# Kernel tuning notes

Measured on AMD Instinct MI355X. Metric: run time of the kernel, lower is better.

Reference implementation:

```python
import jax, jax.numpy as jnp
import numpy as np

N = 2048
EMBED_DIM = 64
N_SUBJ, N_REL, N_OBJ = 16, 9, 16


def setup_inputs() -> dict:
    key = jax.random.key(0)
    ks = jax.random.split(key, 16)
    scale = 0.05  # keep sigmoid unsaturated
    return {
        "subj_idx": jax.random.randint(ks[0], (N,), 0, N_SUBJ, dtype=jnp.int32),
        "rel_idx": jax.random.randint(ks[1], (N,), 0, N_REL, dtype=jnp.int32),
        "obj_idx": jax.random.randint(ks[2], (N,), 0, N_OBJ, dtype=jnp.int32),
        "subj_table": jax.random.normal(ks[3], (N_SUBJ, EMBED_DIM), jnp.float32),
        "rel_table": jax.random.normal(ks[4], (N_REL, EMBED_DIM), jnp.float32),
        "obj_table": jax.random.normal(ks[5], (N_OBJ, EMBED_DIM), jnp.float32),
        "proj_w": jax.random.normal(ks[6], (EMBED_DIM, 3 * EMBED_DIM), jnp.float32) * scale,
        "proj_b": jax.random.normal(ks[7], (EMBED_DIM,), jnp.float32) * scale,
        "w1": jax.random.normal(ks[8], (EMBED_DIM, 2 * EMBED_DIM), jnp.float32) * scale,
        "b1": jax.random.normal(ks[9], (EMBED_DIM,), jnp.float32) * scale,
        "w2": jax.random.normal(ks[10], (32, EMBED_DIM), jnp.float32) * scale,
        "b2": jax.random.normal(ks[11], (32,), jnp.float32) * scale,
        "w3": jax.random.normal(ks[12], (1, 32), jnp.float32) * scale,
        "b3": jax.random.normal(ks[13], (1,), jnp.float32) * scale,
    }


def reference(subj_idx, rel_idx, obj_idx, subj_table, rel_table, obj_table,
              proj_w, proj_b, w1, b1, w2, b2, w3, b3):
    # --- ClaimEmbedder.embed, batched over all N claims ---
    # combined [N, 3*D] = cat(subj, rel, obj) embeddings; proj -> [N, D]
    combined = jnp.concatenate(
        [subj_table[subj_idx], rel_table[rel_idx], obj_table[obj_idx]], axis=-1)
    e = combined @ proj_w.T + proj_b  # [N, D]

    # --- conflict_scorer over all ordered pairs (i, j) ---
    # Linear(2D -> D) on cat(e_i, e_j) == e_i @ W1a.T + e_j @ W1b.T + b1
    d = e.shape[-1]
    w1a, w1b = w1[:, :d], w1[:, d:]
    hi = e @ w1a.T          # [N, D] contribution of left claim
    hj = e @ w1b.T          # [N, D] contribution of right claim
    h = jax.nn.relu(hi[:, None, :] + hj[None, :, :] + b1)  # [N, N, D]
    # Dropout(0.1) is identity in eval / no_grad inference.
    h2 = jax.nn.relu(jnp.einsum('ijd,kd->ijk', h, w2) + b2)  # [N, N, 32]
    scores = jax.nn.sigmoid(jnp.einsum('ijk,k->ij', h2, w3[0]) + b3[0])  # [N, N]
    # Only pairs with i < j are scored in the original nested loop.
    return jnp.triu(scores, k=1)
```

## Files before the change

### kernel.cpp

```cpp
#include <hip/hip_runtime.h>
#include <hip/hip_bf16.h>

#define NROWS 2048
#define HH 72

typedef __attribute__((ext_vector_type(4))) float f32x4;
typedef _Float16 f16x2 __attribute__((ext_vector_type(2)));
typedef _Float16 f16x8 __attribute__((ext_vector_type(8)));
typedef __fp16 fp16x2_raw __attribute__((ext_vector_type(2)));

union H8 { f16x8 v; f16x2 h2[4]; };

static __device__ __forceinline__ f32x4 vmax0(f32x4 a) {
    return __builtin_elementwise_max(a, (f32x4)0.f);
}
static __device__ __forceinline__ f16x8 hmax0(f16x8 a) {
    return __builtin_elementwise_max(a, (f16x8)(_Float16)0.f);
}
static __device__ __forceinline__ f16x2 pkrtz(float a, float b) {
    union { fp16x2_raw r; f16x2 f; } c;
    c.r = __builtin_amdgcn_cvt_pkrtz(a, b);
    return c.f;
}

#define TJ_OFF   2688
#define H16_OFF  5376

__global__ __launch_bounds__(256) void tab_kernel(
    const float* __restrict__ subj_table, const float* __restrict__ rel_table,
    const float* __restrict__ obj_table,
    const float* __restrict__ proj_w, const float* __restrict__ proj_b,
    const float* __restrict__ w1, const float* __restrict__ b1,
    float* __restrict__ ws)
{
    __shared__ float et[64];
    const int b = blockIdx.x;
    const int side = b & 1;
    const int r = b >> 1;
    const int tid = threadIdx.x;
    const int lane = tid & 63;
    const int w = tid >> 6;

    if (r == 41) {
        if (tid < 64) et[tid] = proj_b[tid];
    } else {
        const float* src; int off;
        if (r < 16)      { src = subj_table + r * 64;        off = 0;   }
        else if (r < 25) { src = rel_table + (r - 16) * 64;  off = 64;  }
        else             { src = obj_table + (r - 25) * 64;  off = 128; }
        const float sv = src[lane];
        #pragma unroll
        for (int t = 0; t < 4; ++t) {
            const int d0 = w * 16 + t * 4;
            float p0 = sv * proj_w[(d0 + 0) * 192 + off + lane];
            float p1 = sv * proj_w[(d0 + 1) * 192 + off + lane];
            float p2 = sv * proj_w[(d0 + 2) * 192 + off + lane];
            float p3 = sv * proj_w[(d0 + 3) * 192 + off + lane];
            #pragma unroll
            for (int m = 1; m < 64; m <<= 1) {
                p0 += __shfl_xor(p0, m, 64);
                p1 += __shfl_xor(p1, m, 64);
                p2 += __shfl_xor(p2, m, 64);
                p3 += __shfl_xor(p3, m, 64);
            }
            if (lane == 0) {
                et[d0 + 0] = p0; et[d0 + 1] = p1;
                et[d0 + 2] = p2; et[d0 + 3] = p3;
            }
        }
    }
    __syncthreads();

    float* dst = ws + (side ? TJ_OFF : 0);
    const float sv2 = et[lane];
    const int woff = side * 64;
    #pragma unroll
    for (int t = 0; t < 4; ++t) {
        const int d0 = w * 16 + t * 4;
        float p0 = sv2 * w1[(d0 + 0) * 128 + woff + lane];
        float p1 = sv2 * w1[(d0 + 1) * 128 + woff + lane];
        float p2 = sv2 * w1[(d0 + 2) * 128 + woff + lane];
        float p3 = sv2 * w1[(d0 + 3) * 128 + woff + lane];
        #pragma unroll
        for (int m = 1; m < 64; m <<= 1) {
            p0 += __shfl_xor(p0, m, 64);
            p1 += __shfl_xor(p1, m, 64);
            p2 += __shfl_xor(p2, m, 64);
            p3 += __shfl_xor(p3, m, 64);
        }
        if (lane == 0) {
            const bool cst = (side == 0) && (r == 41);
            dst[r * 64 + d0 + 0] = p0 + (cst ? b1[d0 + 0] : 0.f);
            dst[r * 64 + d0 + 1] = p1 + (cst ? b1[d0 + 1] : 0.f);
            dst[r * 64 + d0 + 2] = p2 + (cst ? b1[d0 + 2] : 0.f);
            dst[r * 64 + d0 + 3] = p3 + (cst ? b1[d0 + 3] : 0.f);
        }
    }
}

__global__ __launch_bounds__(256) void hgather_kernel(
    const int* __restrict__ subj_idx, const int* __restrict__ rel_idx,
    const int* __restrict__ obj_idx, float* __restrict__ ws)
{
    _Float16* hi16 = (_Float16*)(ws + H16_OFF);
    _Float16* hj16 = hi16 + NROWS * 64;
    const float* TI = ws;
    const float* TJ = ws + TJ_OFF;

    const int t = threadIdx.x;
    const int n = blockIdx.x * 32 + (t >> 3);
    const int c = (t & 7) * 8;

    const int s = subj_idx[n];
    const int r = 16 + rel_idx[n];
    const int o = 25 + obj_idx[n];

    const f32x4 v0 = *(const f32x4*)(TI + s * 64 + c)
                   + *(const f32x4*)(TI + r * 64 + c)
                   + *(const f32x4*)(TI + o * 64 + c)
                   + *(const f32x4*)(TI + 41 * 64 + c);
    const f32x4 v1 = *(const f32x4*)(TI + s * 64 + c + 4)
                   + *(const f32x4*)(TI + r * 64 + c + 4)
                   + *(const f32x4*)(TI + o * 64 + c + 4)
                   + *(const f32x4*)(TI + 41 * 64 + c + 4);
    H8 hp;
    hp.h2[0] = pkrtz(v0[0], v0[1]); hp.h2[1] = pkrtz(v0[2], v0[3]);
    hp.h2[2] = pkrtz(v1[0], v1[1]); hp.h2[3] = pkrtz(v1[2], v1[3]);
    *(f16x8*)&hi16[(size_t)n * 64 + c] = hp.v;

    const f32x4 u0 = *(const f32x4*)(TJ + s * 64 + c)
                   + *(const f32x4*)(TJ + r * 64 + c)
                   + *(const f32x4*)(TJ + o * 64 + c)
                   + *(const f32x4*)(TJ + 41 * 64 + c);
    const f32x4 u1 = *(const f32x4*)(TJ + s * 64 + c + 4)
                   + *(const f32x4*)(TJ + r * 64 + c + 4)
                   + *(const f32x4*)(TJ + o * 64 + c + 4)
                   + *(const f32x4*)(TJ + 41 * 64 + c + 4);
    H8 hq;
    hq.h2[0] = pkrtz(u0[0], u0[1]); hq.h2[1] = pkrtz(u0[2], u0[3]);
    hq.h2[2] = pkrtz(u1[0], u1[1]); hq.h2[3] = pkrtz(u1[2], u1[3]);
    *(f16x8*)&hj16[(size_t)n * 64 + c] = hq.v;
}

__global__ __launch_bounds__(256) void zfill_kernel(float* __restrict__ out)
{
    const int bid = blockIdx.x;
    int by = (int)((1.f + sqrtf(1.f + 8.f * (float)bid)) * 0.5f);
    while (by * (by - 1) / 2 > bid) --by;
    while ((by + 1) * by / 2 <= bid) ++by;
    const int bx = bid - by * (by - 1) / 2;
    const int i0 = by * 32, j0 = bx * 32;
    const int t = threadIdx.x;
    const int r = t >> 3, c = (t & 7) * 4;
    const float4 z = {0.f, 0.f, 0.f, 0.f};
    *(float4*)(out + (size_t)(i0 + r) * NROWS + j0 + c) = z;
}

#define PSTR2 132

__global__ __launch_bounds__(256, 4) void pair_kernel(
    const float* __restrict__ ws,
    const float* __restrict__ w2, const float* __restrict__ b2,
    const float* __restrict__ w3, const float* __restrict__ b3,
    float* __restrict__ out)
{
    const int bid = blockIdx.x;
    int by = (int)((129.f - sqrtf(16641.f - 8.f * (float)bid)) * 0.5f);
    while (by * (129 - by) / 2 > bid) --by;
    while ((by + 1) * (129 - (by + 1)) / 2 <= bid) ++by;
    const int bx = by + (bid - by * (129 - by) / 2);
    const int i0 = by * 32, j0 = bx * 32;
    const int tid = threadIdx.x;

    __shared__ _Float16 hiL[32 * HH];
    __shared__ _Float16 hjL[32 * HH];
    __shared__ float part[4 * 8 * PSTR2];

    const _Float16* hi16 = (const _Float16*)(ws + H16_OFF);
    const _Float16* hj16 = hi16 + NROWS * 64;

    const int lane = tid & 63;
    const int wi   = tid >> 6;
    const int col  = lane & 15;
    const int quad = lane >> 4;

    {
        const int rr = tid >> 3;
        const int cc = (tid & 7) * 8;
        *(f16x8*)&hiL[rr * HH + cc] = *(const f16x8*)(hi16 + (size_t)(i0 + rr) * 64 + cc);
        *(f16x8*)&hjL[rr * HH + cc] = *(const f16x8*)(hj16 + (size_t)(j0 + rr) * 64 + cc);
    }

    H8 wf[2][2];
    #pragma unroll
    for (int ch = 0; ch < 2; ++ch)
        #pragma unroll
        for (int ks = 0; ks < 2; ++ks) {
            const f32x4* wr = (const f32x4*)(w2 + (ch * 16 + col) * 64 + ks * 32 + quad * 8);
            const f32x4 w0 = wr[0], w1v = wr[1];
            wf[ch][ks].h2[0] = pkrtz(w0[0], w0[1]);
            wf[ch][ks].h2[1] = pkrtz(w0[2], w0[3]);
            wf[ch][ks].h2[2] = pkrtz(w1v[0], w1v[1]);
            wf[ch][ks].h2[3] = pkrtz(w1v[2], w1v[3]);
        }
    const f32x4 b2A = *(const f32x4*)(b2 + quad * 4);
    const f32x4 b2B = *(const f32x4*)(b2 + 16 + quad * 4);
    const f32x4 w3A = *(const f32x4*)(w3 + quad * 4);
    const f32x4 w3B = *(const f32x4*)(w3 + 16 + quad * 4);
    const float b3v = b3[0];

    __syncthreads();

    const int hjb0 = (col) * HH + quad * 8;
    const int hjb1 = (16 + col) * HH + quad * 8;
    const f16x8 hj00 = *(const f16x8*)&hjL[hjb0];
    const f16x8 hj01 = *(const f16x8*)&hjL[hjb0 + 32];
    const f16x8 hj10 = *(const f16x8*)&hjL[hjb1];
    const f16x8 hj11 = *(const f16x8*)&hjL[hjb1 + 32];

    float* mypart = &part[wi * 8 * PSTR2];

    #pragma unroll
    for (int it = 0; it < 8; ++it) {
        const int base = (wi * 8 + it) * HH + quad * 8;
        const f16x8 x0 = *(const f16x8*)&hiL[base];
        const f16x8 x1 = *(const f16x8*)&hiL[base + 32];

        const f16x8 f00 = hmax0(x0 + hj00);
        const f16x8 f01 = hmax0(x1 + hj01);
        const f16x8 f10 = hmax0(x0 + hj10);
        const f16x8 f11 = hmax0(x1 + hj11);

        f32x4 a0 = __builtin_amdgcn_mfma_f32_16x16x32_f16(wf[0][0].v, f00, b2A, 0, 0, 0);
        f32x4 b0 = __builtin_amdgcn_mfma_f32_16x16x32_f16(wf[1][0].v, f00, b2B, 0, 0, 0);
        f32x4 a1 = __builtin_amdgcn_mfma_f32_16x16x32_f16(wf[0][0].v, f10, b2A, 0, 0, 0);
        f32x4 b1 = __builtin_amdgcn_mfma_f32_16x16x32_f16(wf[1][0].v, f10, b2B, 0, 0, 0);
        a0 = __builtin_amdgcn_mfma_f32_16x16x32_f16(wf[0][1].v, f01, a0, 0, 0, 0);
        b0 = __builtin_amdgcn_mfma_f32_16x16x32_f16(wf[1][1].v, f01, b0, 0, 0, 0);
        a1 = __builtin_amdgcn_mfma_f32_16x16x32_f16(wf[0][1].v, f11, a1, 0, 0, 0);
        b1 = __builtin_amdgcn_mfma_f32_16x16x32_f16(wf[1][1].v, f11, b1, 0, 0, 0);

        const f32x4 t0 = vmax0(a0) * w3A + vmax0(b0) * w3B;
        const f32x4 t1 = vmax0(a1) * w3A + vmax0(b1) * w3B;
        mypart[it * PSTR2 +      quad * 16 + col] = (t0[0] + t0[1]) + (t0[2] + t0[3]);
        mypart[it * PSTR2 + 64 + quad * 16 + col] = (t1[0] + t1[1]) + (t1[2] + t1[3]);
    }

    {
        const int itx = lane >> 3;
        const int jc  = (lane & 7) * 4;
        const int g   = jc >> 4;
        const int c4  = jc & 15;
        const float* pr = &mypart[itx * PSTR2 + g * 64 + c4];
        const f32x4 s = *(const f32x4*)(pr)
                      + *(const f32x4*)(pr + 16)
                      + *(const f32x4*)(pr + 32)
                      + *(const f32x4*)(pr + 48);
        const int i  = i0 + wi * 8 + itx;
        const int jb = j0 + jc;
        float4 o;
        o.x = (jb + 0 > i) ? 1.f / (1.f + __expf(-(s[0] + b3v))) : 0.f;
        o.y = (jb + 1 > i) ? 1.f / (1.f + __expf(-(s[1] + b3v))) : 0.f;
        o.z = (jb + 2 > i) ? 1.f / (1.f + __expf(-(s[2] + b3v))) : 0.f;
        o.w = (jb + 3 > i) ? 1.f / (1.f + __expf(-(s[3] + b3v))) : 0.f;
        *(float4*)(out + (size_t)i * NROWS + jb) = o;
    }
}

extern "C" void kernel_launch(void* const* d_in, const int* in_sizes, int n_in,
                              void* d_out, int out_size, void* d_ws, size_t ws_size,
                              hipStream_t stream) {
    const int*   subj_idx   = (const int*)d_in[0];
    const int*   rel_idx    = (const int*)d_in[1];
    const int*   obj_idx    = (const int*)d_in[2];
    const float* subj_table = (const float*)d_in[3];
    const float* rel_table  = (const float*)d_in[4];
    const float* obj_table  = (const float*)d_in[5];
    const float* proj_w     = (const float*)d_in[6];
    const float* proj_b     = (const float*)d_in[7];
    const float* w1         = (const float*)d_in[8];
    const float* b1         = (const float*)d_in[9];
    const float* w2         = (const float*)d_in[10];
    const float* b2         = (const float*)d_in[11];
    const float* w3         = (const float*)d_in[12];
    const float* b3         = (const float*)d_in[13];
    float* out = (float*)d_out;
    float* ws  = (float*)d_ws;

    zfill_kernel<<<dim3(2016), dim3(256), 0, stream>>>(out);

    tab_kernel<<<dim3(84), dim3(256), 0, stream>>>(
        subj_table, rel_table, obj_table, proj_w, proj_b, w1, b1, ws);

    hgather_kernel<<<dim3(NROWS / 32), dim3(256), 0, stream>>>(
        subj_idx, rel_idx, obj_idx, ws);

    pair_kernel<<<dim3(2080), dim3(256), 0, stream>>>(
        ws, w2, b2, w3, b3, out);
}
```

Measured before the change: 111.9 us.

## Make pair kernel persistent over tiles with register-prefetched next tile

The pair kernel launches 512 blocks instead of 2080, and each block loops over 4 or 5 upper-triangular tiles. It prefetches the next tile's hi/hj rows into registers while computing the current one. This amortizes the per-block weight setup (w2 conversion, bias loads) and hides global load latency, and the launch bound drops to 2 blocks per SM. The cost is extra __syncthreads per tile and fewer blocks to balance load across CUs.

```diff
diff --git a/kernel.cpp b/kernel.cpp
--- a/kernel.cpp
+++ b/kernel.cpp
@@ -21,6 +21,14 @@
     union { fp16x2_raw r; f16x2 f; } c;
     c.r = __builtin_amdgcn_cvt_pkrtz(a, b);
     return c.f;
+}
+
+static __device__ __forceinline__ void decode_tile(int t, int& oby, int& obx) {
+    int b = (int)((129.f - sqrtf(16641.f - 8.f * (float)t)) * 0.5f);
+    while (b * (129 - b) / 2 > t) --b;
+    while ((b + 1) * (129 - (b + 1)) / 2 <= t) ++b;
+    oby = b;
+    obx = b + (t - b * (129 - b) / 2);
 }
 
 #define TJ_OFF   2688
@@ -158,19 +166,15 @@
 
 #define PSTR2 132
 
-__global__ __launch_bounds__(256, 4) void pair_kernel(
+__global__ __launch_bounds__(256, 2) void pair_kernel(
     const float* __restrict__ ws,
     const float* __restrict__ w2, const float* __restrict__ b2,
     const float* __restrict__ w3, const float* __restrict__ b3,
     float* __restrict__ out)
 {
-    const int bid = blockIdx.x;
-    int by = (int)((129.f - sqrtf(16641.f - 8.f * (float)bid)) * 0.5f);
-    while (by * (129 - by) / 2 > bid) --by;
-    while ((by + 1) * (129 - (by + 1)) / 2 <= bid) ++by;
-    const int bx = by + (bid - by * (129 - by) / 2);
-    const int i0 = by * 32, j0 = bx * 32;
+    const int blk = blockIdx.x;
     const int tid = threadIdx.x;
+    const int ntile = 4 + (blk < 32);
 
     __shared__ _Float16 hiL[32 * HH];
     __shared__ _Float16 hjL[32 * HH];
@@ -183,13 +187,8 @@
     const int wi   = tid >> 6;
     const int col  = lane & 15;
     const int quad = lane >> 4;
-
-    {
-        const int rr = tid >> 3;
-        const int cc = (tid & 7) * 8;
-        *(f16x8*)&hiL[rr * HH + cc] = *(const f16x8*)(hi16 + (size_t)(i0 + rr) * 64 + cc);
-        *(f16x8*)&hjL[rr * HH + cc] = *(const f16x8*)(hj16 + (size_t)(j0 + rr) * 64 + cc);
-    }
+    const int rr   = tid >> 3;
+    const int cc   = (tid & 7) * 8;
 
     H8 wf[2][2];
     #pragma unroll
@@ -209,61 +208,83 @@
     const f32x4 w3B = *(const f32x4*)(w3 + 16 + quad * 4);
     const float b3v = b3[0];
 
-    __syncthreads();
-
-    const int hjb0 = (col) * HH + quad * 8;
-    const int hjb1 = (16 + col) * HH + quad * 8;
-    const f16x8 hj00 = *(const f16x8*)&hjL[hjb0];
-    const f16x8 hj01 = *(const f16x8*)&hjL[hjb0 + 32];
-    const f16x8 hj10 = *(const f16x8*)&hjL[hjb1];
-    const f16x8 hj11 = *(const f16x8*)&hjL[hjb1 + 32];
-
     float* mypart = &part[wi * 8 * PSTR2];
 
-    #pragma unroll
-    for (int it = 0; it < 8; ++it) {
-        const int base = (wi * 8 + it) * HH + quad * 8;
-        const f16x8 x0 = *(const f16x8*)&hiL[base];
-        const f16x8 x1 = *(const f16x8*)&hiL[base + 32];
-
-        const f16x8 f00 = hmax0(x0 + hj00);
-        const f16x8 f01 = hmax0(x1 + hj01);
-        const f16x8 f10 = hmax0(x0 + hj10);
-        const f16x8 f11 = hmax0(x1 + hj11);
-
-        f32x4 a0 = __builtin_amdgcn_mfma_f32_16x16x32_f16(wf[0][0].v, f00, b2A, 0, 0, 0);
-        f32x4 b0 = __builtin_amdgcn_mfma_f32_16x16x32_f16(wf[1][0].v, f00, b2B, 0, 0, 0);
-        f32x4 a1 = __builtin_amdgcn_mfma_f32_16x16x32_f16(wf[0][0].v, f10, b2A, 0, 0, 0);
-        f32x4 b1 = __builtin_amdgcn_mfma_f32_16x16x32_f16(wf[1][0].v, f10, b2B, 0, 0, 0);
-        a0 = __builtin_amdgcn_mfma_f32_16x16x32_f16(wf[0][1].v, f01, a0, 0, 0, 0);
-        b0 = __builtin_amdgcn_mfma_f32_16x16x32_f16(wf[1][1].v, f01, b0, 0, 0, 0);
-        a1 = __builtin_amdgcn_mfma_f32_16x16x32_f16(wf[0][1].v, f11, a1, 0, 0, 0);
-        b1 = __builtin_amdgcn_mfma_f32_16x16x32_f16(wf[1][1].v, f11, b1, 0, 0, 0);
-
-        const f32x4 t0 = vmax0(a0) * w3A + vmax0(b0) * w3B;
-        const f32x4 t1 = vmax0(a1) * w3A + vmax0(b1) * w3B;
-        mypart[it * PSTR2 +      quad * 16 + col] = (t0[0] + t0[1]) + (t0[2] + t0[3]);
-        mypart[it * PSTR2 + 64 + quad * 16 + col] = (t1[0] + t1[1]) + (t1[2] + t1[3]);
-    }
-
-    {
-        const int itx = lane >> 3;
-        const int jc  = (lane & 7) * 4;
-        const int g   = jc >> 4;
-        const int c4  = jc & 15;
-        const float* pr = &mypart[itx * PSTR2 + g * 64 + c4];
-        const f32x4 s = *(const f32x4*)(pr)
-                      + *(const f32x4*)(pr + 16)
-                      + *(const f32x4*)(pr + 32)
-                      + *(const f32x4*)(pr + 48);
-        const int i  = i0 + wi * 8 + itx;
-        const int jb = j0 + jc;
-        float4 o;
-        o.x = (jb + 0 > i) ? 1.f / (1.f + __expf(-(s[0] + b3v))) : 0.f;
-        o.y = (jb + 1 > i) ? 1.f / (1.f + __expf(-(s[1] + b3v))) : 0.f;
-        o.z = (jb + 2 > i) ? 1.f / (1.f + __expf(-(s[2] + b3v))) : 0.f;
-        o.w = (jb + 3 > i) ? 1.f / (1.f + __expf(-(s[3] + b3v))) : 0.f;
-        *(float4*)(out + (size_t)i * NROWS + jb) = o;
+    int by, bx;
+    decode_tile(blk * 4, by, bx);
+    f16x8 hiR = *(const f16x8*)(hi16 + (size_t)(by * 32 + rr) * 64 + cc);
+    f16x8 hjR = *(const f16x8*)(hj16 + (size_t)(bx * 32 + rr) * 64 + cc);
+
+    for (int tt = 0; tt < ntile; ++tt) {
+        *(f16x8*)&hiL[rr * HH + cc] = hiR;
+        *(f16x8*)&hjL[rr * HH + cc] = hjR;
+        __syncthreads();
+
+        const int i0 = by * 32, j0 = bx * 32;
+
+        int nby = by, nbx = bx;
+        if (tt + 1 < ntile) {
+            const int tnext = (tt + 1 < 4) ? blk * 4 + tt + 1 : 2048 + blk;
+            decode_tile(tnext, nby, nbx);
+            hiR = *(const f16x8*)(hi16 + (size_t)(nby * 32 + rr) * 64 + cc);
+            hjR = *(const f16x8*)(hj16 + (size_t)(nbx * 32 + rr) * 64 + cc);
+        }
+
+        const int hjb0 = (col) * HH + quad * 8;
+        const int hjb1 = (16 + col) * HH + quad * 8;
+        const f16x8 hj00 = *(const f16x8*)&hjL[hjb0];
+        const f16x8 hj01 = *(const f16x8*)&hjL[hjb0 + 32];
+        const f16x8 hj10 = *(const f16x8*)&hjL[hjb1];
+        const f16x8 hj11 = *(const f16x8*)&hjL[hjb1 + 32];
+
+        #pragma unroll
+        for (int it = 0; it < 8; ++it) {
+            const int base = (wi * 8 + it) * HH + quad * 8;
+            const f16x8 x0 = *(const f16x8*)&hiL[base];
+            const f16x8 x1 = *(const f16x8*)&hiL[base + 32];
+
+            const f16x8 f00 = hmax0(x0 + hj00);
+            const f16x8 f01 = hmax0(x1 + hj01);
+            const f16x8 f10 = hmax0(x0 + hj10);
+            const f16x8 f11 = hmax0(x1 + hj11);
+
+            f32x4 a0 = __builtin_amdgcn_mfma_f32_16x16x32_f16(wf[0][0].v, f00, b2A, 0, 0, 0);
+            f32x4 b0 = __builtin_amdgcn_mfma_f32_16x16x32_f16(wf[1][0].v, f00, b2B, 0, 0, 0);
+            f32x4 a1 = __builtin_amdgcn_mfma_f32_16x16x32_f16(wf[0][0].v, f10, b2A, 0, 0, 0);
+            f32x4 b1 = __builtin_amdgcn_mfma_f32_16x16x32_f16(wf[1][0].v, f10, b2B, 0, 0, 0);
+            a0 = __builtin_amdgcn_mfma_f32_16x16x32_f16(wf[0][1].v, f01, a0, 0, 0, 0);
+            b0 = __builtin_amdgcn_mfma_f32_16x16x32_f16(wf[1][1].v, f01, b0, 0, 0, 0);
+            a1 = __builtin_amdgcn_mfma_f32_16x16x32_f16(wf[0][1].v, f11, a1, 0, 0, 0);
+            b1 = __builtin_amdgcn_mfma_f32_16x16x32_f16(wf[1][1].v, f11, b1, 0, 0, 0);
+
+            const f32x4 t0 = vmax0(a0) * w3A + vmax0(b0) * w3B;
+            const f32x4 t1 = vmax0(a1) * w3A + vmax0(b1) * w3B;
+            mypart[it * PSTR2 +      quad * 16 + col] = (t0[0] + t0[1]) + (t0[2] + t0[3]);
+            mypart[it * PSTR2 + 64 + quad * 16 + col] = (t1[0] + t1[1]) + (t1[2] + t1[3]);
+        }
+
+        {
+            const int itx = lane >> 3;
+            const int jc  = (lane & 7) * 4;
+            const int g   = jc >> 4;
+            const int c4  = jc & 15;
+            const float* pr = &mypart[itx * PSTR2 + g * 64 + c4];
+            const f32x4 s = *(const f32x4*)(pr)
+                          + *(const f32x4*)(pr + 16)
+                          + *(const f32x4*)(pr + 32)
+                          + *(const f32x4*)(pr + 48);
+            const int i  = i0 + wi * 8 + itx;
+            const int jb = j0 + jc;
+            float4 o;
+            o.x = (jb + 0 > i) ? 1.f / (1.f + __expf(-(s[0] + b3v))) : 0.f;
+            o.y = (jb + 1 > i) ? 1.f / (1.f + __expf(-(s[1] + b3v))) : 0.f;
+            o.z = (jb + 2 > i) ? 1.f / (1.f + __expf(-(s[2] + b3v))) : 0.f;
+            o.w = (jb + 3 > i) ? 1.f / (1.f + __expf(-(s[3] + b3v))) : 0.f;
+            *(float4*)(out + (size_t)i * NROWS + jb) = o;
+        }
+
+        __syncthreads();
+        by = nby; bx = nbx;
     }
 }
 
@@ -295,6 +316,6 @@
     hgather_kernel<<<dim3(NROWS / 32), dim3(256), 0, stream>>>(
         subj_idx, rel_idx, obj_idx, ws);
 
-    pair_kernel<<<dim3(2080), dim3(256), 0, stream>>>(
+    pair_kernel<<<dim3(512), dim3(256), 0, stream>>>(
         ws, w2, b2, w3, b3, out);
 }
```

Measured after the change: 112.7 us. About the same (+0.7%).
